# Optimization experiments

Hardware: AMD Instinct MI355X
Metric: run time of the kernel (lower is better)

## Reference

```python
import jax, jax.numpy as jnp
import numpy as np

TEMPERATURE = 10.0
NUM_PROBES = 100


def setup_inputs() -> dict:
    key = jax.random.key(0)
    k1, k2 = jax.random.split(key)
    N, C = 50000, 20
    y_pred = jax.random.normal(k1, (N, C), dtype=jnp.float32)
    s = jax.random.randint(k2, (N,), 0, 2, dtype=jnp.int32)
    return {"y_pred": y_pred, "s": s}


def reference(y_pred, s):
    # y_pred: [N, C], s: [N] in {0,1}
    # Per-class probing grid: 100 points from min to max of that class's preds.
    # torch's .item() detaches min/max from the graph -> stop_gradient here.
    mn = jax.lax.stop_gradient(jnp.min(y_pred, axis=0))  # [C]
    mx = jax.lax.stop_gradient(jnp.max(y_pred, axis=0))  # [C]
    frac = jnp.arange(NUM_PROBES, dtype=y_pred.dtype) / (NUM_PROBES - 1)  # [P]
    grid = mn[:, None] + (mx - mn)[:, None] * frac[None, :]  # [C, P]

    # Smoothed ECDF via sigmoid: diff has shape [C, P, N]
    preds = y_pred.T  # [C, N]
    sig = jax.nn.sigmoid(TEMPERATURE * (grid[:, :, None] - preds[:, None, :]))

    mask0 = (s == 0).astype(y_pred.dtype)  # [N]
    mask1 = (s == 1).astype(y_pred.dtype)
    n0 = jnp.sum(mask0)
    n1 = jnp.sum(mask1)

    # Masked group means == per-group mean since sigmoid is elementwise
    cdf0 = jnp.einsum('cpn,n->cp', sig, mask0) / n0  # [C, P]
    cdf1 = jnp.einsum('cpn,n->cp', sig, mask1) / n1  # [C, P]

    delta = jnp.abs(cdf0 - cdf1)  # [C, P]
    # loss_i = max over probes; final = max over classes -> global max
    return jnp.max(delta)
```

## Files before the change

### kernel.cpp

```cpp
#include <hip/hip_runtime.h>

#define NC 20
#define NP 100
#define PG 10
#define NPG (NP / PG)
#define SLICES 8
#define TPB 256
#define KLOG2E 14.426950408889634f
#define NBS 256

__device__ __forceinline__ float fexp2(float x) {
#if __has_builtin(__builtin_amdgcn_exp2f)
    return __builtin_amdgcn_exp2f(x);
#else
    return __builtin_exp2f(x);
#endif
}
__device__ __forceinline__ float sgpr_f(float x) {
    return __uint_as_float(__builtin_amdgcn_readfirstlane(__float_as_uint(x)));
}

template<bool WRITE_T>
__global__ __launch_bounds__(256)
void prep_kernel(const float* __restrict__ y, const int* __restrict__ s,
                 float* __restrict__ E, float* __restrict__ sf,
                 float* __restrict__ part_mn, float* __restrict__ part_mx,
                 int* __restrict__ part_cnt, int N, int ncap) {
    const int q = blockIdx.y;
    const int bx = blockIdx.x;
    float mn[4] = {3.4e38f, 3.4e38f, 3.4e38f, 3.4e38f};
    float mx[4] = {-3.4e38f, -3.4e38f, -3.4e38f, -3.4e38f};
    int cnt = 0;
    const int stride = gridDim.x * 256;
    for (int n = bx * 256 + threadIdx.x; n < ncap; n += stride) {
        if (n < N) {
            float4 f = ((const float4*)y)[n * 5 + q];
            float v[4] = {f.x, f.y, f.z, f.w};
#pragma unroll
            for (int cc = 0; cc < 4; ++cc) {
                mn[cc] = fminf(mn[cc], v[cc]);
                mx[cc] = fmaxf(mx[cc], v[cc]);
                if (WRITE_T) E[(size_t)(4 * q + cc) * ncap + n] = fexp2(v[cc] * KLOG2E);
            }
            if (q == 0) {
                int m = s[n];
                cnt += m;
                if (WRITE_T) sf[n] = (float)m;
            }
        } else if (WRITE_T) {
#pragma unroll
            for (int cc = 0; cc < 4; ++cc)
                E[(size_t)(4 * q + cc) * ncap + n] = __builtin_inff();
            if (q == 0) sf[n] = 0.f;
        }
    }
#pragma unroll
    for (int off = 1; off < 64; off <<= 1) {
#pragma unroll
        for (int cc = 0; cc < 4; ++cc) {
            mn[cc] = fminf(mn[cc], __shfl_xor(mn[cc], off));
            mx[cc] = fmaxf(mx[cc], __shfl_xor(mx[cc], off));
        }
        cnt += __shfl_xor(cnt, off);
    }
    __shared__ float smn[4][4], smx[4][4];
    __shared__ int scnt[4];
    const int wave = threadIdx.x >> 6, lane = threadIdx.x & 63;
    if (lane == 0) {
#pragma unroll
        for (int cc = 0; cc < 4; ++cc) { smn[wave][cc] = mn[cc]; smx[wave][cc] = mx[cc]; }
        scnt[wave] = cnt;
    }
    __syncthreads();
    const int t = threadIdx.x;
    if (t < 4) {
        part_mn[(4 * q + t) * NBS + bx] =
            fminf(fminf(smn[0][t], smn[1][t]), fminf(smn[2][t], smn[3][t]));
    } else if (t < 8) {
        int cc = t - 4;
        part_mx[(4 * q + cc) * NBS + bx] =
            fmaxf(fmaxf(smx[0][cc], smx[1][cc]), fmaxf(smx[2][cc], smx[3][cc]));
    } else if (t == 8 && q == 0) {
        part_cnt[bx] = scnt[0] + scnt[1] + scnt[2] + scnt[3];
    }
}

template<bool RAW>
__global__ __launch_bounds__(256)
void cdf2_kernel(const float* __restrict__ E, const float* __restrict__ sf,
                 const float* __restrict__ y, const int* __restrict__ s,
                 const float* __restrict__ part_mn, const float* __restrict__ part_mx,
                 const int* __restrict__ part_cnt,
                 float* __restrict__ acc_part, int N, int ncap, int nb) {
    const int c = blockIdx.x;
    const int pg = blockIdx.y;
    float lmn = 3.4e38f, lmx = -3.4e38f;
    int lcnt = 0;
    for (int t = threadIdx.x; t < nb; t += 256) {
        lmn = fminf(lmn, part_mn[c * NBS + t]);
        lmx = fmaxf(lmx, part_mx[c * NBS + t]);
        lcnt += part_cnt[t];
    }
#pragma unroll
    for (int off = 1; off < 64; off <<= 1) {
        lmn = fminf(lmn, __shfl_xor(lmn, off));
        lmx = fmaxf(lmx, __shfl_xor(lmx, off));
        lcnt += __shfl_xor(lcnt, off);
    }
    __shared__ float rmn[4], rmx[4];
    __shared__ int rcnt[4];
    const int wave = threadIdx.x >> 6, lane = threadIdx.x & 63;
    if (lane == 0) { rmn[wave] = lmn; rmx[wave] = lmx; rcnt[wave] = lcnt; }
    __syncthreads();
    const float mn = fminf(fminf(rmn[0], rmn[1]), fminf(rmn[2], rmn[3]));
    const float mx = fmaxf(fmaxf(rmx[0], rmx[1]), fmaxf(rmx[2], rmx[3]));
    const int n1 = rcnt[0] + rcnt[1] + rcnt[2] + rcnt[3];
    const float inv1 = 1.0f / (float)n1;
    const float inv0 = 1.0f / (float)(N - n1);
    const float sA = sgpr_f(inv1 + inv0);
    const float sB = sgpr_f(-inv0);

    int p = pg * PG + (lane % PG);
    float frac = (float)p / 99.0f;
    float g = fmaf(mx - mn, frac, mn);
    float Gl = fexp2(-g * KLOG2E);
    float G[PG];
#pragma unroll
    for (int j = 0; j < PG; ++j) G[j] = sgpr_f(__shfl(Gl, j));

    float d[PG];
#pragma unroll
    for (int j = 0; j < PG; ++j) d[j] = 0.f;

    const int nq = ncap >> 2;
    if (!RAW) {
        const float4* E4 = (const float4*)(E + (size_t)c * ncap);
        const float4* S4 = (const float4*)sf;
        for (int q = blockIdx.z * TPB + threadIdx.x; q < nq; q += TPB * SLICES) {
            float4 ev = E4[q];
            float4 mv = S4[q];
            float ee[4] = {ev.x, ev.y, ev.z, ev.w};
            float ww[4];
            ww[0] = fmaf(mv.x, sA, sB); ww[1] = fmaf(mv.y, sA, sB);
            ww[2] = fmaf(mv.z, sA, sB); ww[3] = fmaf(mv.w, sA, sB);
#pragma unroll
            for (int e = 0; e < 4; ++e) {
#pragma unroll
                for (int j = 0; j < PG; ++j) {
                    float t = fmaf(ee[e], G[j], 1.0f);
                    float r = __builtin_amdgcn_rcpf(t);
                    d[j] = fmaf(r, ww[e], d[j]);
                }
            }
        }
    } else {
        for (int q = blockIdx.z * TPB + threadIdx.x; q < nq; q += TPB * SLICES) {
#pragma unroll
            for (int e = 0; e < 4; ++e) {
                int n = q * 4 + e;
                bool valid = n < N;
                float ev = valid ? fexp2(y[(size_t)n * NC + c] * KLOG2E)
                                 : __builtin_inff();
                float w  = valid ? fmaf((float)s[n], sA, sB) : 0.f;
#pragma unroll
                for (int j = 0; j < PG; ++j) {
                    float t = fmaf(ev, G[j], 1.0f);
                    float r = __builtin_amdgcn_rcpf(t);
                    d[j] = fmaf(r, w, d[j]);
                }
            }
        }
    }
#pragma unroll
    for (int off = 1; off < 64; off <<= 1) {
#pragma unroll
        for (int j = 0; j < PG; ++j) d[j] += __shfl_xor(d[j], off);
    }
    __shared__ float sd[4][PG];
    if (lane == 0) {
#pragma unroll
        for (int j = 0; j < PG; ++j) sd[wave][j] = d[j];
    }
    __syncthreads();
    if (threadIdx.x < PG) {
        int j = threadIdx.x;
        float v = (sd[0][j] + sd[1][j]) + (sd[2][j] + sd[3][j]);
        acc_part[(size_t)(c * NP + pg * PG + j) * SLICES + blockIdx.z] = v;
    }
}

__global__ __launch_bounds__(256)
void finalize_kernel(const float* __restrict__ acc_part, float* __restrict__ out) {
    float m = 0.f;
    for (int i = threadIdx.x; i < NC * NP; i += 256) {
        const float4* p4 = (const float4*)(acc_part + (size_t)i * SLICES);
        float4 a = p4[0], b = p4[1];
        float ssum = ((a.x + a.y) + (a.z + a.w)) + ((b.x + b.y) + (b.z + b.w));
        m = fmaxf(m, fabsf(ssum));
    }
#pragma unroll
    for (int off = 1; off < 64; off <<= 1)
        m = fmaxf(m, __shfl_xor(m, off));
    __shared__ float red[4];
    const int wave = threadIdx.x >> 6, lane = threadIdx.x & 63;
    if (lane == 0) red[wave] = m;
    __syncthreads();
    if (threadIdx.x == 0)
        out[0] = fmaxf(fmaxf(red[0], red[1]), fmaxf(red[2], red[3]));
}

extern "C" void kernel_launch(void* const* d_in, const int* in_sizes, int n_in,
                              void* d_out, int out_size, void* d_ws, size_t ws_size,
                              hipStream_t stream) {
    const float* y = (const float*)d_in[0];
    const int* s   = (const int*)d_in[1];
    const int N = in_sizes[1];
    const int ncap = ((N + 1023) / 1024) * 1024;
    int nb = ncap / 256;
    if (nb > NBS) nb = NBS;

    unsigned char* ws = (unsigned char*)d_ws;
    float* part_mn = (float*)ws;
    float* part_mx = (float*)(ws + 20480);
    int*   part_cnt= (int*)  (ws + 40960);
    float* acc_part= (float*)(ws + 45056);
    float* E       = (float*)(ws + 131072);
    float* sf      = (float*)(ws + 131072 + (size_t)4 * NC * ncap);
    size_t need = 131072 + (size_t)4 * (NC + 1) * ncap;
    bool fat = ws_size >= need;

    dim3 gA(nb, 5);
    if (fat) prep_kernel<true ><<<gA, 256, 0, stream>>>(y, s, E, sf, part_mn, part_mx, part_cnt, N, ncap);
    else     prep_kernel<false><<<gA, 256, 0, stream>>>(y, s, nullptr, nullptr, part_mn, part_mx, part_cnt, N, ncap);

    dim3 gB(NC, NPG, SLICES);
    if (fat) cdf2_kernel<false><<<gB, 256, 0, stream>>>(E, sf, y, s, part_mn, part_mx, part_cnt, acc_part, N, ncap, nb);
    else     cdf2_kernel<true ><<<gB, 256, 0, stream>>>(nullptr, nullptr, y, s, part_mn, part_mx, part_cnt, acc_part, N, ncap, nb);

    finalize_kernel<<<1, 256, 0, stream>>>(acc_part, (float*)d_out);
}
```

Baseline: 33.18 us.

## Fuse finalize into cdf kernel via atomics and last-block reduction

Drops the separate finalize launch. Each cdf block now atomically adds its per-probe partial sums into a zeroed accumulator, and the last block to finish (found with an agent-scope counter) computes the global max. The accumulator and counter are zeroed inside the prep kernel. SLICES also rises from 8 to 10 for more blocks. This removes one kernel launch and its gap, at the cost of float atomics (nondeterministic summation order) and counter contention.

```diff
diff --git a/kernel.cpp b/kernel.cpp
--- a/kernel.cpp
+++ b/kernel.cpp
@@ -4,10 +4,11 @@
 #define NP 100
 #define PG 10
 #define NPG (NP / PG)
-#define SLICES 8
+#define SLICES 10
 #define TPB 256
 #define KLOG2E 14.426950408889634f
 #define NBS 256
+#define NBLK (NC * NPG * SLICES)
 
 __device__ __forceinline__ float fexp2(float x) {
 #if __has_builtin(__builtin_amdgcn_exp2f)
@@ -25,9 +26,16 @@
 void prep_kernel(const float* __restrict__ y, const int* __restrict__ s,
                  float* __restrict__ E, float* __restrict__ sf,
                  float* __restrict__ part_mn, float* __restrict__ part_mx,
-                 int* __restrict__ part_cnt, int N, int ncap) {
+                 int* __restrict__ part_cnt, float* __restrict__ acc_d,
+                 unsigned* __restrict__ done_cnt, int N, int ncap) {
     const int q = blockIdx.y;
     const int bx = blockIdx.x;
+    if (q == 1 && bx < 8) {
+        int zi = bx * 256 + threadIdx.x;
+        if (zi < NC * NP) acc_d[zi] = 0.f;
+    }
+    if (q == 2 && bx == 0 && threadIdx.x == 0) *done_cnt = 0u;
+
     float mn[4] = {3.4e38f, 3.4e38f, 3.4e38f, 3.4e38f};
     float mx[4] = {-3.4e38f, -3.4e38f, -3.4e38f, -3.4e38f};
     int cnt = 0;
@@ -91,7 +99,8 @@
                  const float* __restrict__ y, const int* __restrict__ s,
                  const float* __restrict__ part_mn, const float* __restrict__ part_mx,
                  const int* __restrict__ part_cnt,
-                 float* __restrict__ acc_part, int N, int ncap, int nb) {
+                 float* __restrict__ acc_d, unsigned* __restrict__ done_cnt,
+                 float* __restrict__ out, int N, int ncap, int nb) {
     const int c = blockIdx.x;
     const int pg = blockIdx.y;
     float lmn = 3.4e38f, lmx = -3.4e38f;
@@ -185,24 +194,27 @@
     if (threadIdx.x < PG) {
         int j = threadIdx.x;
         float v = (sd[0][j] + sd[1][j]) + (sd[2][j] + sd[3][j]);
-        acc_part[(size_t)(c * NP + pg * PG + j) * SLICES + blockIdx.z] = v;
-    }
-}
-
-__global__ __launch_bounds__(256)
-void finalize_kernel(const float* __restrict__ acc_part, float* __restrict__ out) {
+        atomicAdd(&acc_d[c * NP + pg * PG + j], v);
+    }
+    __shared__ int is_last;
+    if (threadIdx.x == 0) {
+        unsigned prev = __hip_atomic_fetch_add(done_cnt, 1u, __ATOMIC_ACQ_REL,
+                                               __HIP_MEMORY_SCOPE_AGENT);
+        is_last = (prev == NBLK - 1);
+    }
+    __syncthreads();
+    if (!is_last) return;
+
     float m = 0.f;
     for (int i = threadIdx.x; i < NC * NP; i += 256) {
-        const float4* p4 = (const float4*)(acc_part + (size_t)i * SLICES);
-        float4 a = p4[0], b = p4[1];
-        float ssum = ((a.x + a.y) + (a.z + a.w)) + ((b.x + b.y) + (b.z + b.w));
-        m = fmaxf(m, fabsf(ssum));
+        float v = __hip_atomic_load(&acc_d[i], __ATOMIC_RELAXED,
+                                    __HIP_MEMORY_SCOPE_AGENT);
+        m = fmaxf(m, fabsf(v));
     }
 #pragma unroll
     for (int off = 1; off < 64; off <<= 1)
         m = fmaxf(m, __shfl_xor(m, off));
     __shared__ float red[4];
-    const int wave = threadIdx.x >> 6, lane = threadIdx.x & 63;
     if (lane == 0) red[wave] = m;
     __syncthreads();
     if (threadIdx.x == 0)
@@ -220,22 +232,21 @@
     if (nb > NBS) nb = NBS;
 
     unsigned char* ws = (unsigned char*)d_ws;
-    float* part_mn = (float*)ws;
-    float* part_mx = (float*)(ws + 20480);
-    int*   part_cnt= (int*)  (ws + 40960);
-    float* acc_part= (float*)(ws + 45056);
-    float* E       = (float*)(ws + 131072);
-    float* sf      = (float*)(ws + 131072 + (size_t)4 * NC * ncap);
+    float* part_mn  = (float*)ws;
+    float* part_mx  = (float*)(ws + 20480);
+    int*   part_cnt = (int*)  (ws + 40960);
+    unsigned* done  = (unsigned*)(ws + 41984);
+    float* acc_d    = (float*)(ws + 45056);
+    float* E        = (float*)(ws + 131072);
+    float* sf       = (float*)(ws + 131072 + (size_t)4 * NC * ncap);
     size_t need = 131072 + (size_t)4 * (NC + 1) * ncap;
     bool fat = ws_size >= need;
 
     dim3 gA(nb, 5);
-    if (fat) prep_kernel<true ><<<gA, 256, 0, stream>>>(y, s, E, sf, part_mn, part_mx, part_cnt, N, ncap);
-    else     prep_kernel<false><<<gA, 256, 0, stream>>>(y, s, nullptr, nullptr, part_mn, part_mx, part_cnt, N, ncap);
+    if (fat) prep_kernel<true ><<<gA, 256, 0, stream>>>(y, s, E, sf, part_mn, part_mx, part_cnt, acc_d, done, N, ncap);
+    else     prep_kernel<false><<<gA, 256, 0, stream>>>(y, s, nullptr, nullptr, part_mn, part_mx, part_cnt, acc_d, done, N, ncap);
 
     dim3 gB(NC, NPG, SLICES);
-    if (fat) cdf2_kernel<false><<<gB, 256, 0, stream>>>(E, sf, y, s, part_mn, part_mx, part_cnt, acc_part, N, ncap, nb);
-    else     cdf2_kernel<true ><<<gB, 256, 0, stream>>>(nullptr, nullptr, y, s, part_mn, part_mx, part_cnt, acc_part, N, ncap, nb);
-
-    finalize_kernel<<<1, 256, 0, stream>>>(acc_part, (float*)d_out);
-}
+    if (fat) cdf2_kernel<false><<<gB, 256, 0, stream>>>(E, sf, y, s, part_mn, part_mx, part_cnt, acc_d, done, (float*)d_out, N, ncap, nb);
+    else     cdf2_kernel<true ><<<gB, 256, 0, stream>>>(nullptr, nullptr, y, s, part_mn, part_mx, part_cnt, acc_d, done, (float*)d_out, N, ncap, nb);
+}
```

Result: slower. 65.90 us (+98.6%).
